# Kernel tuning notes

Hardware: AMD Instinct MI355X
Metric: run time of the kernel (lower is better)

## Reference

```python
import jax, jax.numpy as jnp
import numpy as np

B, L, H, SH, C = 32, 512, 1024, 50, 3   # batch, leaves, hidden, hidden_syn_size, num_classes
N = 2 * L - 1                            # total tree nodes (complete binary / heap order)
VOCAB, SYN = 30000, 128
LVLS = int(np.log2(L))                   # number of internal levels (root = level 0)


def _linear(k, fin, fout):
    lim = 1.0 / np.sqrt(fin)
    kw, kb = jax.random.split(k)
    W = jax.random.uniform(kw, (fin, fout), minval=-lim, maxval=lim, dtype=jnp.float32)
    b = jax.random.uniform(kb, (fout,), minval=-lim, maxval=lim, dtype=jnp.float32)
    return W, b


def setup_inputs() -> dict:
    key = jax.random.key(0)
    ks = jax.random.split(key, 12)
    x = jax.random.randint(ks[0], (B, N), 0, SYN)                 # node ids (word at leaves, syntax elsewhere)
    word_index = jnp.broadcast_to(jnp.arange(L - 1, 2 * L - 1), (B, L))  # leaf node indices (heap order)
    cue = jax.random.randint(ks[1], (B, N), 0, C)
    pos = jax.random.randint(ks[2], (B, L), 0, SYN)               # POS tag per leaf
    # parent->child adjacency of the heap tree, adj[:,1] is what forward reads
    A = np.zeros((N, N), dtype=bool)
    par = np.arange(L - 1)
    A[par, 2 * par + 1] = True
    A[par, 2 * par + 2] = True
    adj = jnp.broadcast_to(jnp.asarray(A)[None, None], (B, 2, N, N))
    pre_embs = jnp.zeros((1,), jnp.float32)                       # unused (use_pretrained_embs=False)
    word_emb_W = jax.random.normal(ks[3], (VOCAB, H), jnp.float32) * 0.02
    syn_emb_W = jax.random.normal(ks[4], (SYN, SH), jnp.float32) * 0.02
    leaf_W, leaf_b = _linear(ks[5], H + SH + C, H)
    comp_W, comp_b = _linear(ks[6], 2 * H + SH, H)
    grev_W, grev_b = _linear(ks[7], H + SH, H)
    dec_W, dec_b = _linear(ks[8], 2 * H + 2 * SH, 2 * H)
    clf_W, clf_b = _linear(ks[9], 2 * H, C)
    return dict(x=x, word_index=word_index, cue=cue, adj=adj, pos=pos, pre_embs=pre_embs,
                word_emb_W=word_emb_W, syn_emb_W=syn_emb_W,
                leaf_W=leaf_W, leaf_b=leaf_b, comp_W=comp_W, comp_b=comp_b,
                grev_W=grev_W, grev_b=grev_b, dec_W=dec_W, dec_b=dec_b,
                clf_W=clf_W, clf_b=clf_b)


def reference(x, word_index, cue, adj, pos, pre_embs,
              word_emb_W, syn_emb_W, leaf_W, leaf_b, comp_W, comp_b,
              grev_W, grev_b, dec_W, dec_b, clf_W, clf_b):
    # Eval-mode forward (self.training == False, so no dropout masks are applied).
    # Tree structure is the complete binary heap encoded in adj: children of i are 2i+1, 2i+2.
    b_ix = jnp.arange(B)[:, None]
    s = jnp.take_along_axis(x, word_index, axis=1)                # (B,L) leaf word ids
    c = jnp.take_along_axis(cue, word_index, axis=1)              # (B,L) leaf cue ids
    word_e = word_emb_W[s]                                        # (B,L,H)
    cue_e = jax.nn.one_hot(c, C, dtype=word_e.dtype)              # (B,L,C)
    pos_e = syn_emb_W[pos]                                        # (B,L,SH)
    x_emb = jnp.concatenate([word_e, cue_e, pos_e], -1) @ leaf_W + leaf_b  # (B,L,H), no activation

    up = jnp.zeros((B, N, H), x_emb.dtype).at[b_ix, word_index].set(x_emb)
    # upward pass: batched level-order compose (bottom internal level -> root)
    for lvl in range(LVLS - 1, -1, -1):
        nodes = jnp.arange(2 ** lvl - 1, 2 ** (lvl + 1) - 1)
        l, r = 2 * nodes + 1, 2 * nodes + 2
        cons = syn_emb_W[x[:, nodes]]                             # (B,W,SH)
        ctx = jnp.concatenate([cons, up[:, l], up[:, r]], -1)     # (B,W,SH+2H)
        up = up.at[:, nodes].set(jnp.tanh(ctx @ comp_W + comp_b))

    root_ctx = jnp.concatenate([up[:, 0], syn_emb_W[x[:, 0]]], -1)
    gd = jnp.tanh(root_ctx @ grev_W + grev_b)                     # (B,H)
    down = jnp.zeros((B, N, H), gd.dtype).at[:, 0].set(gd)
    # downward pass: batched level-order decompose (root -> leaves)
    for lvl in range(LVLS):
        nodes = jnp.arange(2 ** lvl - 1, 2 ** (lvl + 1) - 1)
        l, r = 2 * nodes + 1, 2 * nodes + 2
        if lvl == LVLS - 1:   # children are leaves -> their syntax is the POS embedding
            cons_l = pos_e[:, l - (L - 1)]
            cons_r = pos_e[:, r - (L - 1)]
        else:
            cons_l = syn_emb_W[x[:, l]]
            cons_r = syn_emb_W[x[:, r]]
        pctx = jnp.concatenate([down[:, nodes], up[:, nodes]], -1)  # (parent_emb, upward[parent])
        dctx = jnp.concatenate([cons_l, cons_r, pctx], -1)
        ch = jnp.tanh(dctx @ dec_W + dec_b)                        # (B,W,2H)
        down = down.at[:, l].set(ch[..., :H]).at[:, r].set(ch[..., H:])

    tree = jnp.concatenate([down, up], -1)                         # (B,N,2H)
    return jnp.tanh(tree @ clf_W + clf_b)                          # (B,N,C)
```

## Files before the change

### kernel.cpp

```cpp
#include <hip/hip_runtime.h>

typedef unsigned short u16;
typedef unsigned int   u32;

typedef __bf16 bf16x8 __attribute__((ext_vector_type(8)));
typedef float  f32x4  __attribute__((ext_vector_type(4)));

#define NB 1023
#define HH 1024

__device__ __forceinline__ float b2f(u16 x) { return __uint_as_float(((u32)x) << 16); }
__device__ __forceinline__ u16 f2b(float f) {
    u32 u = __float_as_uint(f);
    u += 0x7fffu + ((u >> 16) & 1u);
    return (u16)(u >> 16);
}
__device__ __forceinline__ float fast_tanh(float x) {
    float cx = fminf(fmaxf(x, -12.f), 12.f);
    float e = __expf(2.f * cx);
    return __fdividef(e - 1.f, e + 1.f);
}
__device__ __forceinline__ void async_copy16(const void* gptr, void* lptr) {
    __builtin_amdgcn_global_load_lds((__attribute__((address_space(1))) void*)gptr,
                                     (__attribute__((address_space(3))) void*)lptr,
                                     16, 0, 0);
}
__device__ __forceinline__ u16 loadAsBf16(const void* p, size_t idx, int isf32) {
    if (isf32) return f2b(((const float*)p)[idx]);
    return ((const u16*)p)[idx];
}

__device__ __forceinline__ int detect_local(const u32* __restrict__ w) {
    __shared__ int cnt;
    const int tid = threadIdx.x;
    if (tid == 0) cnt = 0;
    __syncthreads();
    u32 v = w[tid & 255];
    u32 lo = v & 0xFFFFu;
    u32 e = (lo >> 7) & 0xFFu;
    if ((lo != 0u) && (e < 60u || e > 140u)) atomicAdd(&cnt, 1);
    __syncthreads();
    return cnt >= 64;
}

__device__ void conv_range(const void* __restrict__ src, u16* __restrict__ dst,
                           int n, int tbase, int isf32) {
    const int i = ((int)blockIdx.x - tbase) * 256 + threadIdx.x;
    if (i < n) dst[i] = loadAsBf16(src, i, isf32);
}

__device__ void transpose_tile(const void* __restrict__ W, u16* __restrict__ Wt,
                               int Nw, int Kpad, int bx, int by, int isf32,
                               int ps0, int ps1, int ps2, int ps3,
                               int os0, int os1, int os2, int os3,
                               int ln0, int ln1, int ln2, int ln3)
{
    __shared__ u16 tile[32][33];
    const int tid = threadIdx.x;
    const int tx = tid & 31, ty = tid >> 5;
    #pragma unroll
    for (int i = 0; i < 4; ++i) {
        const int kp = by*32 + ty + i*8;
        const int n = bx*32 + tx;
        int ko = -1;
        if      (kp >= ps0 && kp < ps0 + ln0) ko = os0 + (kp - ps0);
        else if (kp >= ps1 && kp < ps1 + ln1) ko = os1 + (kp - ps1);
        else if (kp >= ps2 && kp < ps2 + ln2) ko = os2 + (kp - ps2);
        else if (kp >= ps3 && kp < ps3 + ln3) ko = os3 + (kp - ps3);
        u16 v = 0;
        if (ko >= 0) v = loadAsBf16(W, (size_t)ko * Nw + n, isf32);
        tile[ty + i*8][tx] = v;
    }
    __syncthreads();
    #pragma unroll
    for (int i = 0; i < 4; ++i) {
        const int n = bx*32 + ty + i*8;
        const int kp = by*32 + tx;
        Wt[(size_t)n * Kpad + kp] = tile[tx][ty + i*8];
    }
}

__global__ __launch_bounds__(256)
void preprocess(const u32* __restrict__ wembU,
                const void* __restrict__ semb,  const void* __restrict__ leafb,
                const void* __restrict__ compb, const void* __restrict__ grevb,
                const void* __restrict__ decb,  const void* __restrict__ clfb,
                const void* __restrict__ clfW,
                const void* __restrict__ leafW, const void* __restrict__ compW,
                const void* __restrict__ grevW, const void* __restrict__ decW,
                u16* __restrict__ sembP,  u16* __restrict__ leafbC,
                u16* __restrict__ compbC, u16* __restrict__ grevbC,
                u16* __restrict__ decbC,  u16* __restrict__ clfbC,
                u16* __restrict__ clfWC,
                u16* __restrict__ leafWt, u16* __restrict__ compWt,
                u16* __restrict__ grevWt, u16* __restrict__ decWt)
{
    const int isf32 = detect_local(wembU);
    const int bid = blockIdx.x;
    if (bid < 32) {
        const int i = bid * 256 + threadIdx.x;
        const int s = i >> 6, c = i & 63;
        sembP[i] = (c < 50) ? loadAsBf16(semb, s * 50 + c, isf32) : (u16)0;
    } else if (bid < 36)  conv_range(leafb, leafbC, 1024, 32, isf32);
    else if (bid < 40)  conv_range(compb, compbC, 1024, 36, isf32);
    else if (bid < 44)  conv_range(grevb, grevbC, 1024, 40, isf32);
    else if (bid < 52)  conv_range(decb,  decbC,  2048, 44, isf32);
    else if (bid < 53)  conv_range(clfb,  clfbC,  3,    52, isf32);
    else if (bid < 77)  conv_range(clfW,  clfWC,  6144, 53, isf32);
    else if (bid < 1165) {
        const int t = bid - 77;
        transpose_tile(leafW, leafWt, 1024, 1088, t & 31, t >> 5, isf32,
                       0,-1,-1,-1,  0,0,0,0,  1077,0,0,0);
    } else if (bid < 3277) {
        const int t = bid - 1165;
        transpose_tile(compW, compWt, 1024, 2112, t & 31, t >> 5, isf32,
                       0,64,1088,-1,  0,50,1074,0,  50,1024,1024,0);
    } else if (bid < 4365) {
        const int t = bid - 3277;
        transpose_tile(grevW, grevWt, 1024, 1088, t & 31, t >> 5, isf32,
                       0,1024,-1,-1,  0,1024,0,0,  1024,50,0,0);
    } else {
        const int t = bid - 4365;
        transpose_tile(decW, decWt, 2048, 2176, t & 63, t >> 6, isf32,
                       0,64,128,1152,  0,50,100,1124,  50,50,1024,1024);
    }
}

__global__ __launch_bounds__(256)
void leaf_gather(const int* __restrict__ x, const int* __restrict__ cue,
                 const int* __restrict__ pos, const void* __restrict__ wemb,
                 const u16* __restrict__ sembP, u16* __restrict__ ctx)
{
    const int isf32 = detect_local((const u32*)wemb);
    const int m = blockIdx.x;
    const int b = m >> 9, i = m & 511;
    const int node = 511 + i;
    const int s  = x[b*NB + node];
    const int cv = cue[b*NB + node];
    const int p  = pos[b*512 + i];
    u16* row = ctx + (size_t)m * 1088;
    u32* row32 = (u32*)row;
    const u16* sr = sembP + p * 64;
    const int tid = threadIdx.x;
    if (isf32) {
        const float2* wrf = ((const float2*)wemb) + (size_t)s * 512;
        for (int c = tid; c < 512; c += 256) {
            float2 t = wrf[c];
            row32[c] = (u32)f2b(t.x) | ((u32)f2b(t.y) << 16);
        }
    } else {
        const u32* wr = ((const u32*)wemb) + (size_t)s * 512;
        for (int c = tid; c < 512; c += 256) row32[c] = wr[c];
    }
    if (tid < 64) {
        const int c = tid;
        u16 v;
        if (c < 3)       v = (c == cv) ? (u16)0x3F80 : (u16)0;
        else if (c < 53) v = sr[c - 3];
        else             v = 0;
        row[1024 + c] = v;
    }
}

template<int AKIND, int MODE>
__global__ __launch_bounds__(256)
void gemm_fused(const u16* __restrict__ Bt, const u16* __restrict__ bias,
                u16* __restrict__ dst, int M, int Kpad, int nodeBase, int lognn,
                int leafLvl,
                const u16* __restrict__ actx,
                const int* __restrict__ x, const int* __restrict__ pos,
                const u16* __restrict__ sembP,
                const u16* __restrict__ upB, const u16* __restrict__ downB)
{
    __shared__ __align__(16) u16 As[2*4096];
    __shared__ __align__(16) u16 Bs[2*4096];
    const int tid  = threadIdx.x;
    const int wave = tid >> 6;
    const int lane = tid & 63;
    const int bm = blockIdx.y << 7;
    const int bn = blockIdx.x << 7;
    const int wm = (wave & 1) << 6;
    const int wn = (wave >> 1) << 6;
    const int quad = lane >> 4;
    const int l16  = lane & 15;
    const int srow = lane >> 2;
    const int scol = (lane & 3) << 3;
    const int mask = (1 << lognn) - 1;

    const u16* p0[2]; const u16* p1[2]; const u16* p2[2]; const u16* p3[2];
    #pragma unroll
    for (int h = 0; h < 2; ++h) {
        const int mrow = bm + wave*16 + srow + h*64;
        const int mr = (mrow < M) ? mrow : 0;
        if (AKIND == 0) {
            p0[h] = actx + (size_t)mr * Kpad + scol;
        } else if (AKIND == 1) {
            const int b_ = mr >> lognn, ii = mr & mask;
            const int node = nodeBase + ii;
            const int s = x[b_*NB + node];
            p0[h] = sembP + s*64 + scol;
            p1[h] = upB + (((size_t)(b_*NB + 2*node + 1)) << 10) + scol;
            p2[h] = upB + (((size_t)(b_*NB + 2*node + 2)) << 10) + scol;
        } else if (AKIND == 2) {
            p0[h] = upB + (((size_t)(mr*NB)) << 10) + scol;
            p1[h] = sembP + x[mr*NB]*64 + scol;
        } else {
            const int b_ = mr >> lognn, ii = mr & mask;
            const int node = nodeBase + ii;
            const int l = 2*node + 1, r = l + 1;
            int sli, sri;
            if (leafLvl) { sli = pos[b_*512 + (l-511)]; sri = pos[b_*512 + (r-511)]; }
            else         { sli = x[b_*NB + l]; sri = x[b_*NB + r]; }
            p0[h] = sembP + sli*64 + scol;
            p1[h] = sembP + sri*64 + scol;
            p2[h] = downB + (((size_t)(b_*NB + node)) << 10) + scol;
            p3[h] = upB   + (((size_t)(b_*NB + node)) << 10) + scol;
        }
    }

    const u16* gB0 = Bt + (size_t)(bn + wave*16 + srow) * Kpad + scol;
    const u16* gB1 = gB0 + (size_t)64 * Kpad;
    u16* lA0 = &As[wave * 512];
    u16* lA1 = &As[(wave + 4) * 512];
    u16* lB0 = &Bs[wave * 512];
    u16* lB1 = &Bs[(wave + 4) * 512];

    const u16* pa[4]; const u16* pb[4];
    #pragma unroll
    for (int i = 0; i < 4; ++i) pa[i] = &As[(wm + i*16 + l16) * 32 + quad*8];
    #pragma unroll
    for (int j = 0; j < 4; ++j) pb[j] = &Bs[(wn + j*16 + l16) * 32 + quad*8];

    f32x4 zero4 = {0.f, 0.f, 0.f, 0.f};
    f32x4 acc[4][4];
    #pragma unroll
    for (int i = 0; i < 4; ++i)
        #pragma unroll
        for (int j = 0; j < 4; ++j) acc[i][j] = zero4;

    auto kstep64 = [&](const u16* sA0, const u16* sA1, int k0) {
        async_copy16(sA0,           lA0);
        async_copy16(sA1,           lA1);
        async_copy16(gB0 + k0,      lB0);
        async_copy16(gB1 + k0,      lB1);
        async_copy16(sA0 + 32,      lA0 + 4096);
        async_copy16(sA1 + 32,      lA1 + 4096);
        async_copy16(gB0 + k0 + 32, lB0 + 4096);
        async_copy16(gB1 + k0 + 32, lB1 + 4096);
        __syncthreads();
        #pragma unroll
        for (int c = 0; c < 2; ++c) {
            bf16x8 a[4], b[4];
            #pragma unroll
            for (int i = 0; i < 4; ++i) a[i] = *(const bf16x8*)(pa[i] + c*4096);
            #pragma unroll
            for (int j = 0; j < 4; ++j) b[j] = *(const bf16x8*)(pb[j] + c*4096);
            #pragma unroll
            for (int i = 0; i < 4; ++i)
                #pragma unroll
                for (int j = 0; j < 4; ++j)
                    acc[i][j] = __builtin_amdgcn_mfma_f32_16x16x32_bf16(a[i], b[j], acc[i][j], 0, 0, 0);
        }
        __syncthreads();
    };

    if (AKIND == 0) {
        for (int k0 = 0; k0 < 1088; k0 += 64) kstep64(p0[0] + k0, p0[1] + k0, k0);
    } else if (AKIND == 1) {
        kstep64(p0[0], p0[1], 0);
        for (int k0 = 64;   k0 < 1088; k0 += 64) kstep64(p1[0] + (k0-64),   p1[1] + (k0-64),   k0);
        for (int k0 = 1088; k0 < 2112; k0 += 64) kstep64(p2[0] + (k0-1088), p2[1] + (k0-1088), k0);
    } else if (AKIND == 2) {
        for (int k0 = 0; k0 < 1024; k0 += 64) kstep64(p0[0] + k0, p0[1] + k0, k0);
        kstep64(p1[0], p1[1], 1024);
    } else {
        kstep64(p0[0], p0[1], 0);
        kstep64(p1[0], p1[1], 64);
        for (int k0 = 128;  k0 < 1152; k0 += 64) kstep64(p2[0] + (k0-128),  p2[1] + (k0-128),  k0);
        for (int k0 = 1152; k0 < 2176; k0 += 64) kstep64(p3[0] + (k0-1152), p3[1] + (k0-1152), k0);
    }

    #pragma unroll
    for (int i = 0; i < 4; ++i) {
        #pragma unroll
        for (int j = 0; j < 4; ++j) {
            const int gn = bn + wn + j*16 + l16;
            const float bv = b2f(bias[gn]);
            #pragma unroll
            for (int r = 0; r < 4; ++r) {
                const int gm = bm + wm + i*16 + quad*4 + r;
                if (gm < M) {
                    float v = acc[i][j][r] + bv;
                    if (MODE != 0) v = fast_tanh(v);
                    const int b_ = gm >> lognn;
                    const int ii = gm & mask;
                    const int node = nodeBase + ii;
                    size_t addr;
                    if (MODE == 2) {
                        const int child = 2*node + 1 + (gn >> 10);
                        addr = (((size_t)(b_*NB + child)) << 10) + (gn & 1023);
                    } else {
                        addr = (((size_t)(b_*NB + node)) << 10) + gn;
                    }
                    dst[addr] = f2b(v);
                }
            }
        }
    }
}

__global__ __launch_bounds__(256)
void classifier_kernel(const u16* __restrict__ down, const u16* __restrict__ up,
                       const u16* __restrict__ clfW, const u16* __restrict__ clfb,
                       void* __restrict__ outp, const u32* __restrict__ wembU)
{
    __shared__ float wls[3][2048];
    const int isf32 = detect_local(wembU);
    const int tid = threadIdx.x;
    for (int idx = tid; idx < 6144; idx += 256) {
        const int c = idx >> 11, k = idx & 2047;
        wls[c][k] = b2f(clfW[k*3 + c]);
    }
    __syncthreads();
    const int wave = tid >> 6, lane = tid & 63;
    const float b0 = b2f(clfb[0]), b1 = b2f(clfb[1]), b2v = b2f(clfb[2]);
    const int base = blockIdx.x * 32;
    for (int rr = 0; rr < 8; ++rr) {
        const int row = base + rr*4 + wave;
        const u32* dn = (const u32*)(down + ((size_t)row << 10));
        const u32* un = (const u32*)(up   + ((size_t)row << 10));
        float a0 = 0.f, a1 = 0.f, a2 = 0.f;
        #pragma unroll
        for (int t = 0; t < 8; ++t) {
            const int j = t*64 + lane;
            const u32 dp = dn[j], uu = un[j];
            const int k = j*2;
            const float d0 = __uint_as_float(dp << 16);
            const float d1 = __uint_as_float(dp & 0xffff0000u);
            const float u0 = __uint_as_float(uu << 16);
            const float u1 = __uint_as_float(uu & 0xffff0000u);
            a0 += d0*wls[0][k] + d1*wls[0][k+1] + u0*wls[0][1024+k] + u1*wls[0][1025+k];
            a1 += d0*wls[1][k] + d1*wls[1][k+1] + u0*wls[1][1024+k] + u1*wls[1][1025+k];
            a2 += d0*wls[2][k] + d1*wls[2][k+1] + u0*wls[2][1024+k] + u1*wls[2][1025+k];
        }
        #pragma unroll
        for (int off = 32; off; off >>= 1) {
            a0 += __shfl_down(a0, off);
            a1 += __shfl_down(a1, off);
            a2 += __shfl_down(a2, off);
        }
        if (lane == 0) {
            const float v0 = fast_tanh(a0 + b0);
            const float v1 = fast_tanh(a1 + b1);
            const float v2 = fast_tanh(a2 + b2v);
            if (isf32) {
                float* o = (float*)outp + (size_t)row * 3;
                o[0] = v0; o[1] = v1; o[2] = v2;
            } else {
                u16* o = (u16*)outp + (size_t)row * 3;
                o[0] = f2b(v0); o[1] = f2b(v1); o[2] = f2b(v2);
            }
        }
    }
}

extern "C" void kernel_launch(void* const* d_in, const int* in_sizes, int n_in,
                              void* d_out, int out_size, void* d_ws, size_t ws_size,
                              hipStream_t stream)
{
    (void)in_sizes; (void)n_in; (void)out_size; (void)ws_size;
    const int* x    = (const int*)d_in[0];
    const int* cue  = (const int*)d_in[2];
    const int* pos  = (const int*)d_in[4];
    const void* wemb  = d_in[6];
    const void* semb  = d_in[7];
    const void* leafW = d_in[8];
    const void* leafb = d_in[9];
    const void* compW = d_in[10];
    const void* compb = d_in[11];
    const void* grevW = d_in[12];
    const void* grevb = d_in[13];
    const void* decW  = d_in[14];
    const void* decb  = d_in[15];
    const void* clfW  = d_in[16];
    const void* clfb  = d_in[17];

    char* ws = (char*)d_ws;
    u16* up_buf   = (u16*)(ws + 0);
    u16* down_buf = (u16*)(ws + 67043328);
    u16* ctx      = (u16*)(ws + 134086656);
    u16* leafWt   = (u16*)(ws + 169738240);
    u16* compWt   = (u16*)(ws + 171966464);
    u16* grevWt   = (u16*)(ws + 176291840);
    u16* decWt    = (u16*)(ws + 178520064);
    u16* sembP    = (u16*)(ws + 187432960);
    u16* leafbC   = (u16*)(ws + 187449344);
    u16* compbC   = (u16*)(ws + 187451392);
    u16* grevbC   = (u16*)(ws + 187453440);
    u16* decbC    = (u16*)(ws + 187455488);
    u16* clfbC    = (u16*)(ws + 187459584);
    u16* clfWC    = (u16*)(ws + 187459600);

    preprocess<<<8717, 256, 0, stream>>>((const u32*)wemb,
        semb, leafb, compb, grevb, decb, clfb, clfW,
        leafW, compW, grevW, decW,
        sembP, leafbC, compbC, grevbC, decbC, clfbC, clfWC,
        leafWt, compWt, grevWt, decWt);

    leaf_gather<<<16384, 256, 0, stream>>>(x, cue, pos, wemb, sembP, ctx);
    gemm_fused<0,0><<<dim3(8, 128), 256, 0, stream>>>(leafWt, leafbC, up_buf,
        16384, 1088, 511, 9, 0, ctx, x, pos, sembP, up_buf, down_buf);
    for (int lvl = 8; lvl >= 0; --lvl) {
        const int M = 32 << lvl;
        const int Mpad = M < 128 ? 128 : M;
        const int first = (1 << lvl) - 1;
        gemm_fused<1,1><<<dim3(8, Mpad >> 7), 256, 0, stream>>>(compWt, compbC, up_buf,
            M, 2112, first, lvl, 0, nullptr, x, pos, sembP, up_buf, down_buf);
    }
    gemm_fused<2,1><<<dim3(8, 1), 256, 0, stream>>>(grevWt, grevbC, down_buf,
        32, 1088, 0, 0, 0, nullptr, x, pos, sembP, up_buf, down_buf);
    for (int lvl = 0; lvl <= 8; ++lvl) {
        const int M = 32 << lvl;
        const int Mpad = M < 128 ? 128 : M;
        const int first = (1 << lvl) - 1;
        gemm_fused<3,2><<<dim3(16, Mpad >> 7), 256, 0, stream>>>(decWt, decbC, down_buf,
            M, 2176, first, lvl, lvl == 8 ? 1 : 0, nullptr, x, pos, sembP, up_buf, down_buf);
    }
    classifier_kernel<<<1023, 256, 0, stream>>>(down_buf, up_buf, clfWC, clfbC,
                                                d_out, (const u32*)wemb);
}
```

Before: 1.292 ms.

## Fuse small tree levels into cooperative persistent kernel with double-buffered K loop

The small upward, root and downward tree levels now run in one cooperative kernel of 256 workgroups that separates levels with grid-wide syncs, replacing many small launches. The large levels (comp level 8, decomp levels 7 and 8) stay as separate launches. The GEMM tile loop is restructured into a 32-wide K pipeline that prefetches the next stage while computing the current one, and workgroup IDs are remapped across XCDs. This trades per-launch overhead and tail latency for grid-sync cost, and keeps a fallback path of separate launches if the cooperative launch fails.

```diff
diff --git a/kernel.cpp b/kernel.cpp
--- a/kernel.cpp
+++ b/kernel.cpp
@@ -1,4 +1,7 @@
 #include <hip/hip_runtime.h>
+#include <hip/hip_cooperative_groups.h>
+
+namespace cg = cooperative_groups;
 
 typedef unsigned short u16;
 typedef unsigned int   u32;
@@ -163,22 +166,20 @@
 }
 
 template<int AKIND, int MODE>
-__global__ __launch_bounds__(256)
-void gemm_fused(const u16* __restrict__ Bt, const u16* __restrict__ bias,
-                u16* __restrict__ dst, int M, int Kpad, int nodeBase, int lognn,
-                int leafLvl,
-                const u16* __restrict__ actx,
-                const int* __restrict__ x, const int* __restrict__ pos,
-                const u16* __restrict__ sembP,
-                const u16* __restrict__ upB, const u16* __restrict__ downB)
-{
-    __shared__ __align__(16) u16 As[2*4096];
-    __shared__ __align__(16) u16 Bs[2*4096];
+__device__ __forceinline__ void tile_body(
+    u16* __restrict__ As, u16* __restrict__ Bs,
+    const u16* __restrict__ Bt, const u16* __restrict__ bias,
+    u16* __restrict__ dst, int M, int Kpad, int nodeBase, int lognn,
+    int leafLvl,
+    const u16* __restrict__ actx,
+    const int* __restrict__ x, const int* __restrict__ pos,
+    const u16* __restrict__ sembP,
+    const u16* __restrict__ upB, const u16* __restrict__ downB,
+    int bm, int bn)
+{
     const int tid  = threadIdx.x;
     const int wave = tid >> 6;
     const int lane = tid & 63;
-    const int bm = blockIdx.y << 7;
-    const int bn = blockIdx.x << 7;
     const int wm = (wave & 1) << 6;
     const int wn = (wave >> 1) << 6;
     const int quad = lane >> 4;
@@ -220,16 +221,16 @@
 
     const u16* gB0 = Bt + (size_t)(bn + wave*16 + srow) * Kpad + scol;
     const u16* gB1 = gB0 + (size_t)64 * Kpad;
-    u16* lA0 = &As[wave * 512];
-    u16* lA1 = &As[(wave + 4) * 512];
-    u16* lB0 = &Bs[wave * 512];
-    u16* lB1 = &Bs[(wave + 4) * 512];
+    u16* lA0 = As + wave * 512;
+    u16* lA1 = As + (wave + 4) * 512;
+    u16* lB0 = Bs + wave * 512;
+    u16* lB1 = Bs + (wave + 4) * 512;
 
     const u16* pa[4]; const u16* pb[4];
     #pragma unroll
-    for (int i = 0; i < 4; ++i) pa[i] = &As[(wm + i*16 + l16) * 32 + quad*8];
-    #pragma unroll
-    for (int j = 0; j < 4; ++j) pb[j] = &Bs[(wn + j*16 + l16) * 32 + quad*8];
+    for (int i = 0; i < 4; ++i) pa[i] = As + (wm + i*16 + l16) * 32 + quad*8;
+    #pragma unroll
+    for (int j = 0; j < 4; ++j) pb[j] = Bs + (wn + j*16 + l16) * 32 + quad*8;
 
     f32x4 zero4 = {0.f, 0.f, 0.f, 0.f};
     f32x4 acc[4][4];
@@ -238,46 +239,43 @@
         #pragma unroll
         for (int j = 0; j < 4; ++j) acc[i][j] = zero4;
 
-    auto kstep64 = [&](const u16* sA0, const u16* sA1, int k0) {
-        async_copy16(sA0,           lA0);
-        async_copy16(sA1,           lA1);
-        async_copy16(gB0 + k0,      lB0);
-        async_copy16(gB1 + k0,      lB1);
-        async_copy16(sA0 + 32,      lA0 + 4096);
-        async_copy16(sA1 + 32,      lA1 + 4096);
-        async_copy16(gB0 + k0 + 32, lB0 + 4096);
-        async_copy16(gB1 + k0 + 32, lB1 + 4096);
+    auto srcA = [&](int h, int k0) -> const u16* {
+        if (AKIND == 0) return p0[h] + k0;
+        if (AKIND == 1) return (k0 < 64) ? p0[h] + k0
+                             : (k0 < 1088) ? p1[h] + (k0 - 64)
+                             : p2[h] + (k0 - 1088);
+        if (AKIND == 2) return (k0 < 1024) ? p0[h] + k0 : p1[h] + (k0 - 1024);
+        return (k0 < 64)   ? p0[h] + k0
+             : (k0 < 128)  ? p1[h] + (k0 - 64)
+             : (k0 < 1152) ? p2[h] + (k0 - 128)
+             : p3[h] + (k0 - 1152);
+    };
+    auto stage = [&](int c) {
+        const int off = (c & 1) << 12;
+        const int k0  = c << 5;
+        async_copy16(srcA(0, k0), lA0 + off);
+        async_copy16(srcA(1, k0), lA1 + off);
+        async_copy16(gB0 + k0,    lB0 + off);
+        async_copy16(gB1 + k0,    lB1 + off);
+    };
+
+    const int NT = Kpad >> 5;
+    stage(0);
+    __syncthreads();
+    for (int c = 0; c < NT; ++c) {
+        if (c + 1 < NT) stage(c + 1);
+        const int off = (c & 1) << 12;
+        bf16x8 a[4], b[4];
+        #pragma unroll
+        for (int i = 0; i < 4; ++i) a[i] = *(const bf16x8*)(pa[i] + off);
+        #pragma unroll
+        for (int j = 0; j < 4; ++j) b[j] = *(const bf16x8*)(pb[j] + off);
+        #pragma unroll
+        for (int i = 0; i < 4; ++i)
+            #pragma unroll
+            for (int j = 0; j < 4; ++j)
+                acc[i][j] = __builtin_amdgcn_mfma_f32_16x16x32_bf16(a[i], b[j], acc[i][j], 0, 0, 0);
         __syncthreads();
-        #pragma unroll
-        for (int c = 0; c < 2; ++c) {
-            bf16x8 a[4], b[4];
-            #pragma unroll
-            for (int i = 0; i < 4; ++i) a[i] = *(const bf16x8*)(pa[i] + c*4096);
-            #pragma unroll
-            for (int j = 0; j < 4; ++j) b[j] = *(const bf16x8*)(pb[j] + c*4096);
-            #pragma unroll
-            for (int i = 0; i < 4; ++i)
-                #pragma unroll
-                for (int j = 0; j < 4; ++j)
-                    acc[i][j] = __builtin_amdgcn_mfma_f32_16x16x32_bf16(a[i], b[j], acc[i][j], 0, 0, 0);
-        }
-        __syncthreads();
-    };
-
-    if (AKIND == 0) {
-        for (int k0 = 0; k0 < 1088; k0 += 64) kstep64(p0[0] + k0, p0[1] + k0, k0);
-    } else if (AKIND == 1) {
-        kstep64(p0[0], p0[1], 0);
-        for (int k0 = 64;   k0 < 1088; k0 += 64) kstep64(p1[0] + (k0-64),   p1[1] + (k0-64),   k0);
-        for (int k0 = 1088; k0 < 2112; k0 += 64) kstep64(p2[0] + (k0-1088), p2[1] + (k0-1088), k0);
-    } else if (AKIND == 2) {
-        for (int k0 = 0; k0 < 1024; k0 += 64) kstep64(p0[0] + k0, p0[1] + k0, k0);
-        kstep64(p1[0], p1[1], 1024);
-    } else {
-        kstep64(p0[0], p0[1], 0);
-        kstep64(p1[0], p1[1], 64);
-        for (int k0 = 128;  k0 < 1152; k0 += 64) kstep64(p2[0] + (k0-128),  p2[1] + (k0-128),  k0);
-        for (int k0 = 1152; k0 < 2176; k0 += 64) kstep64(p3[0] + (k0-1152), p3[1] + (k0-1152), k0);
     }
 
     #pragma unroll
@@ -309,6 +307,74 @@
     }
 }
 
+template<int AKIND, int MODE>
+__global__ __launch_bounds__(256)
+void gemm_fused(const u16* __restrict__ Bt, const u16* __restrict__ bias,
+                u16* __restrict__ dst, int M, int Kpad, int nodeBase, int lognn,
+                int leafLvl,
+                const u16* __restrict__ actx,
+                const int* __restrict__ x, const int* __restrict__ pos,
+                const u16* __restrict__ sembP,
+                const u16* __restrict__ upB, const u16* __restrict__ downB)
+{
+    __shared__ __align__(16) u16 As[8192];
+    __shared__ __align__(16) u16 Bs[8192];
+    const int gx  = gridDim.x;
+    const int nwg = gx * gridDim.y;
+    int bid = blockIdx.y * gx + blockIdx.x;
+    const int q = nwg >> 3, r = nwg & 7;
+    const int xcd = bid & 7, lid = bid >> 3;
+    bid = (xcd < r ? xcd * (q + 1) : r * (q + 1) + (xcd - r) * q) + lid;
+    const int bx = bid % gx, by = bid / gx;
+    tile_body<AKIND, MODE>(As, Bs, Bt, bias, dst, M, Kpad, nodeBase, lognn,
+                           leafLvl, actx, x, pos, sembP, upB, downB,
+                           by << 7, bx << 7);
+}
+
+__global__ __launch_bounds__(256)
+void tree_chain(const u16* __restrict__ compWt, const u16* __restrict__ compbC,
+                const u16* __restrict__ grevWt, const u16* __restrict__ grevbC,
+                const u16* __restrict__ decWt,  const u16* __restrict__ decbC,
+                const int* __restrict__ x, const int* __restrict__ pos,
+                const u16* __restrict__ sembP,
+                u16* __restrict__ upB, u16* __restrict__ downB)
+{
+    __shared__ __align__(16) u16 As[8192];
+    __shared__ __align__(16) u16 Bs[8192];
+    cg::grid_group grid = cg::this_grid();
+    const int bid = blockIdx.x;
+
+    for (int lvl = 7; lvl >= 0; --lvl) {
+        const int M = 32 << lvl;
+        const int Mpad = M < 128 ? 128 : M;
+        const int ntile = (Mpad >> 7) * 8;
+        if (bid < ntile) {
+            const int bx = bid & 7, by = bid >> 3;
+            tile_body<1,1>(As, Bs, compWt, compbC, upB, M, 2112, (1 << lvl) - 1,
+                           lvl, 0, nullptr, x, pos, sembP, upB, downB,
+                           by << 7, bx << 7);
+        }
+        grid.sync();
+    }
+    if (bid < 8) {
+        tile_body<2,1>(As, Bs, grevWt, grevbC, downB, 32, 1088, 0, 0, 0,
+                       nullptr, x, pos, sembP, upB, downB, 0, bid << 7);
+    }
+    grid.sync();
+    for (int lvl = 0; lvl <= 6; ++lvl) {
+        const int M = 32 << lvl;
+        const int Mpad = M < 128 ? 128 : M;
+        const int ntile = (Mpad >> 7) * 16;
+        if (bid < ntile) {
+            const int bx = bid & 15, by = bid >> 4;
+            tile_body<3,2>(As, Bs, decWt, decbC, downB, M, 2176, (1 << lvl) - 1,
+                           lvl, 0, nullptr, x, pos, sembP, upB, downB,
+                           by << 7, bx << 7);
+        }
+        grid.sync();
+    }
+}
+
 __global__ __launch_bounds__(256)
 void classifier_kernel(const u16* __restrict__ down, const u16* __restrict__ up,
                        const u16* __restrict__ clfW, const u16* __restrict__ clfb,
@@ -410,22 +476,44 @@
     leaf_gather<<<16384, 256, 0, stream>>>(x, cue, pos, wemb, sembP, ctx);
     gemm_fused<0,0><<<dim3(8, 128), 256, 0, stream>>>(leafWt, leafbC, up_buf,
         16384, 1088, 511, 9, 0, ctx, x, pos, sembP, up_buf, down_buf);
-    for (int lvl = 8; lvl >= 0; --lvl) {
-        const int M = 32 << lvl;
-        const int Mpad = M < 128 ? 128 : M;
-        const int first = (1 << lvl) - 1;
-        gemm_fused<1,1><<<dim3(8, Mpad >> 7), 256, 0, stream>>>(compWt, compbC, up_buf,
-            M, 2112, first, lvl, 0, nullptr, x, pos, sembP, up_buf, down_buf);
-    }
-    gemm_fused<2,1><<<dim3(8, 1), 256, 0, stream>>>(grevWt, grevbC, down_buf,
-        32, 1088, 0, 0, 0, nullptr, x, pos, sembP, up_buf, down_buf);
-    for (int lvl = 0; lvl <= 8; ++lvl) {
-        const int M = 32 << lvl;
-        const int Mpad = M < 128 ? 128 : M;
-        const int first = (1 << lvl) - 1;
-        gemm_fused<3,2><<<dim3(16, Mpad >> 7), 256, 0, stream>>>(decWt, decbC, down_buf,
-            M, 2176, first, lvl, lvl == 8 ? 1 : 0, nullptr, x, pos, sembP, up_buf, down_buf);
-    }
+    gemm_fused<1,1><<<dim3(8, 64), 256, 0, stream>>>(compWt, compbC, up_buf,
+        8192, 2112, 255, 8, 0, nullptr, x, pos, sembP, up_buf, down_buf);
+
+    const u16* compWt_c = compWt; const u16* compbC_c = compbC;
+    const u16* grevWt_c = grevWt; const u16* grevbC_c = grevbC;
+    const u16* decWt_c  = decWt;  const u16* decbC_c  = decbC;
+    const u16* sembP_c  = sembP;
+    void* args[] = {(void*)&compWt_c, (void*)&compbC_c, (void*)&grevWt_c,
+                    (void*)&grevbC_c, (void*)&decWt_c,  (void*)&decbC_c,
+                    (void*)&x, (void*)&pos, (void*)&sembP_c,
+                    (void*)&up_buf, (void*)&down_buf};
+    hipError_t ce = hipLaunchCooperativeKernel((const void*)tree_chain,
+                                               dim3(256), dim3(256), args, 0, stream);
+    if (ce != hipSuccess) {
+        (void)hipGetLastError();
+        for (int lvl = 7; lvl >= 0; --lvl) {
+            const int M = 32 << lvl;
+            const int Mpad = M < 128 ? 128 : M;
+            const int first = (1 << lvl) - 1;
+            gemm_fused<1,1><<<dim3(8, Mpad >> 7), 256, 0, stream>>>(compWt, compbC, up_buf,
+                M, 2112, first, lvl, 0, nullptr, x, pos, sembP, up_buf, down_buf);
+        }
+        gemm_fused<2,1><<<dim3(8, 1), 256, 0, stream>>>(grevWt, grevbC, down_buf,
+            32, 1088, 0, 0, 0, nullptr, x, pos, sembP, up_buf, down_buf);
+        for (int lvl = 0; lvl <= 6; ++lvl) {
+            const int M = 32 << lvl;
+            const int Mpad = M < 128 ? 128 : M;
+            const int first = (1 << lvl) - 1;
+            gemm_fused<3,2><<<dim3(16, Mpad >> 7), 256, 0, stream>>>(decWt, decbC, down_buf,
+                M, 2176, first, lvl, 0, nullptr, x, pos, sembP, up_buf, down_buf);
+        }
+    }
+
+    gemm_fused<3,2><<<dim3(16, 32), 256, 0, stream>>>(decWt, decbC, down_buf,
+        4096, 2176, 127, 7, 0, nullptr, x, pos, sembP, up_buf, down_buf);
+    gemm_fused<3,2><<<dim3(16, 64), 256, 0, stream>>>(decWt, decbC, down_buf,
+        8192, 2176, 255, 8, 1, nullptr, x, pos, sembP, up_buf, down_buf);
+
     classifier_kernel<<<1023, 256, 0, stream>>>(down_buf, up_buf, clfWC, clfbC,
                                                 d_out, (const u32*)wemb);
 }
```

Measured after the change: 1.899 ms. +46.9%, slower.
